# Performance work log

Hardware: AMD Instinct MI355X
Metric: run time of the kernel (lower is better)

The kernel has to match this reference:

```python
import jax, jax.numpy as jnp
import numpy as np

MAX_LEN = 366

def _pe_table(d_model, max_len=MAX_LEN):
    # standard sinusoidal positional encoding table [max_len, d_model]
    pos = jnp.arange(max_len, dtype=jnp.float32)[:, None]
    div = jnp.exp(jnp.arange(0, d_model, 2, dtype=jnp.float32) * (-jnp.log(10000.0) / d_model))
    ang = pos * div  # [max_len, d_model/2]
    pe = jnp.zeros((max_len, d_model), dtype=jnp.float32)
    pe = pe.at[:, 0::2].set(jnp.sin(ang))
    pe = pe.at[:, 1::2].set(jnp.cos(ang))
    return pe

def setup_inputs() -> dict:
    key = jax.random.key(0)
    k1, k2, k3, k4 = jax.random.split(key, 4)
    B, S, F, D = 1024, 128, 10, 256
    input_sequence = jax.random.normal(k1, (B, S, F), dtype=jnp.float32)
    doy_sequence = jnp.sort(jax.random.randint(k2, (B, S), 0, MAX_LEN), axis=-1)
    W = jax.random.normal(k3, (D, F), dtype=jnp.float32) * (1.0 / np.sqrt(F))
    b = jax.random.normal(k4, (D,), dtype=jnp.float32) * 0.01
    return {"input_sequence": input_sequence, "doy_sequence": doy_sequence, "W": W, "b": b}

def reference(input_sequence, doy_sequence, W, b):
    # obs_embed: linear projection of per-observation features  [B,S,D]
    obs_embed = jnp.einsum('bsf,df->bsd', input_sequence, W) + b
    D = W.shape[0]
    pe = _pe_table(D)[doy_sequence]  # vectorized gather over the whole batch [B,S,D]
    # original: x = obs_embed.repeat(1,1,2) then overwrite second half with PE
    out = jnp.concatenate([obs_embed, pe], axis=-1)  # [B,S,2D]
    # dropout is identity in eval mode
    return out
```

## Files before the change

kernel.cpp:

```cpp
#include <hip/hip_runtime.h>


__global__ __launch_bounds__(256) void bert_embed_kernel(
    const float* __restrict__ x,
    const int*   __restrict__ doy,
    const float* __restrict__ W,
    const float* __restrict__ bvec,
    float*       __restrict__ out,
    int BS)
{
    const int lane = threadIdx.x & 63;
    const int wave = threadIdx.x >> 6;
    const int p = blockIdx.x * 4 + wave;
    if (p >= BS) return;

    const float2* xp = (const float2*)(x + (size_t)p * 10);
    float xf[10];
    #pragma unroll
    for (int c = 0; c < 5; ++c) {
        float2 v = xp[c];
        xf[2 * c]     = v.x;
        xf[2 * c + 1] = v.y;
    }

    const int d0 = lane * 4;

    float4 bv = *(const float4*)(bvec + d0);
    float acc[4] = {bv.x, bv.y, bv.z, bv.w};

    {
        const float4* wp = (const float4*)(W + (size_t)d0 * 10);
        float wf[40];
        #pragma unroll
        for (int c = 0; c < 10; ++c) {
            float4 v = wp[c];
            wf[4 * c + 0] = v.x; wf[4 * c + 1] = v.y;
            wf[4 * c + 2] = v.z; wf[4 * c + 3] = v.w;
        }
        #pragma unroll
        for (int r = 0; r < 4; ++r) {
            #pragma unroll
            for (int f = 0; f < 10; ++f)
                acc[r] = fmaf(xf[f], wf[10 * r + f], acc[r]);
        }
    }

    const float pos = (float)doy[p];
    float pe[4];
    #pragma unroll
    for (int q = 0; q < 2; ++q) {
        float j = (float)(2 * lane + q);
        float e = __builtin_amdgcn_exp2f(
            fmaf(j, -0.10381025296522976f, -2.651496129472319f));
        float rev = pos * e;
        float fr = rev - floorf(rev);
        pe[2 * q]     = __builtin_amdgcn_sinf(fr);
        pe[2 * q + 1] = __builtin_amdgcn_cosf(fr);
    }

    float* o = out + (size_t)p * 512;
    float4 s0 = {acc[0], acc[1], acc[2], acc[3]};
    float4 s1 = {pe[0],  pe[1],  pe[2],  pe[3]};
    *(float4*)(o + d0)       = s0;
    *(float4*)(o + 256 + d0) = s1;
}

extern "C" void kernel_launch(void* const* d_in, const int* in_sizes, int n_in,
                              void* d_out, int out_size, void* d_ws, size_t ws_size,
                              hipStream_t stream) {
    const float* x    = (const float*)d_in[0];
    const int*   doy  = (const int*)d_in[1];
    const float* W    = (const float*)d_in[2];
    const float* bvec = (const float*)d_in[3];
    float*       out  = (float*)d_out;

    const int BS = in_sizes[1];
    const int blocks = (BS + 3) / 4;
    bert_embed_kernel<<<blocks, 256, 0, stream>>>(x, doy, W, bvec, out, BS);
}
```

Measured before the change: 318.5 us.

## Process 32 positions per wave, reusing W, bias and PE frequencies in registers

Each wavefront now handles a chunk of 32 consecutive positions instead of one. The W slice, bias and the two exponential frequency terms are loaded or computed once and kept in registers across the chunk. The doy values are loaded in one coalesced read and handed out with shuffles. This cuts redundant W loads and per-position setup, but it shrinks the grid by 32x (about 1024 blocks) and serializes the writes within each wave, which may lower memory-level parallelism on this write-bound kernel.

Result: faster. 280.4 us (-12.0%).

```diff
diff --git a/kernel.cpp b/kernel.cpp
--- a/kernel.cpp
+++ b/kernel.cpp
@@ -1,5 +1,7 @@
 #include <hip/hip_runtime.h>
 
+
+#define CHUNK 32
 
 __global__ __launch_bounds__(256) void bert_embed_kernel(
     const float* __restrict__ x,
@@ -11,58 +13,70 @@
 {
     const int lane = threadIdx.x & 63;
     const int wave = threadIdx.x >> 6;
-    const int p = blockIdx.x * 4 + wave;
-    if (p >= BS) return;
-
-    const float2* xp = (const float2*)(x + (size_t)p * 10);
-    float xf[10];
-    #pragma unroll
-    for (int c = 0; c < 5; ++c) {
-        float2 v = xp[c];
-        xf[2 * c]     = v.x;
-        xf[2 * c + 1] = v.y;
-    }
+    const int gw   = blockIdx.x * 4 + wave;
+    const int base = gw * CHUNK;
+    if (base >= BS) return;
 
     const int d0 = lane * 4;
 
-    float4 bv = *(const float4*)(bvec + d0);
-    float acc[4] = {bv.x, bv.y, bv.z, bv.w};
-
+    float wf[40];
     {
         const float4* wp = (const float4*)(W + (size_t)d0 * 10);
-        float wf[40];
         #pragma unroll
         for (int c = 0; c < 10; ++c) {
             float4 v = wp[c];
             wf[4 * c + 0] = v.x; wf[4 * c + 1] = v.y;
             wf[4 * c + 2] = v.z; wf[4 * c + 3] = v.w;
         }
-        #pragma unroll
-        for (int r = 0; r < 4; ++r) {
-            #pragma unroll
-            for (int f = 0; f < 10; ++f)
-                acc[r] = fmaf(xf[f], wf[10 * r + f], acc[r]);
-        }
     }
 
-    const float pos = (float)doy[p];
-    float pe[4];
-    #pragma unroll
-    for (int q = 0; q < 2; ++q) {
-        float j = (float)(2 * lane + q);
-        float e = __builtin_amdgcn_exp2f(
-            fmaf(j, -0.10381025296522976f, -2.651496129472319f));
-        float rev = pos * e;
-        float fr = rev - floorf(rev);
-        pe[2 * q]     = __builtin_amdgcn_sinf(fr);
-        pe[2 * q + 1] = __builtin_amdgcn_cosf(fr);
+    const float4 bv = *(const float4*)(bvec + d0);
+
+    const float e0 = __builtin_amdgcn_exp2f(
+        fmaf((float)(2 * lane + 0), -0.10381025296522976f, -2.651496129472319f));
+    const float e1 = __builtin_amdgcn_exp2f(
+        fmaf((float)(2 * lane + 1), -0.10381025296522976f, -2.651496129472319f));
+
+    int myDoy = 0;
+    if (lane < CHUNK && base + lane < BS) myDoy = doy[base + lane];
+
+    const int n = min(CHUNK, BS - base);
+    float* o = out + (size_t)base * 512 + d0;
+
+    for (int it = 0; it < n; ++it) {
+        const int p = base + it;
+
+        const float2* xp = (const float2*)(x + (size_t)p * 10);
+        float xf[10];
+        #pragma unroll
+        for (int c = 0; c < 5; ++c) {
+            float2 v = xp[c];
+            xf[2 * c]     = v.x;
+            xf[2 * c + 1] = v.y;
+        }
+
+        float acc0 = bv.x, acc1 = bv.y, acc2 = bv.z, acc3 = bv.w;
+        #pragma unroll
+        for (int f = 0; f < 10; ++f) {
+            acc0 = fmaf(xf[f], wf[ 0 + f], acc0);
+            acc1 = fmaf(xf[f], wf[10 + f], acc1);
+            acc2 = fmaf(xf[f], wf[20 + f], acc2);
+            acc3 = fmaf(xf[f], wf[30 + f], acc3);
+        }
+
+        const float pos = (float)__shfl(myDoy, it);
+        float r0 = pos * e0;
+        float r1 = pos * e1;
+        r0 -= floorf(r0);
+        r1 -= floorf(r1);
+        float4 s1 = { __builtin_amdgcn_sinf(r0), __builtin_amdgcn_cosf(r0),
+                      __builtin_amdgcn_sinf(r1), __builtin_amdgcn_cosf(r1) };
+        float4 s0 = { acc0, acc1, acc2, acc3 };
+
+        *(float4*)(o)       = s0;
+        *(float4*)(o + 256) = s1;
+        o += 512;
     }
-
-    float* o = out + (size_t)p * 512;
-    float4 s0 = {acc[0], acc[1], acc[2], acc[3]};
-    float4 s1 = {pe[0],  pe[1],  pe[2],  pe[3]};
-    *(float4*)(o + d0)       = s0;
-    *(float4*)(o + 256 + d0) = s1;
 }
 
 extern "C" void kernel_launch(void* const* d_in, const int* in_sizes, int n_in,
@@ -75,6 +89,7 @@
     float*       out  = (float*)d_out;
 
     const int BS = in_sizes[1];
-    const int blocks = (BS + 3) / 4;
+    const int waves  = (BS + CHUNK - 1) / CHUNK;
+    const int blocks = (waves + 3) / 4;
     bert_embed_kernel<<<blocks, 256, 0, stream>>>(x, doy, W, bvec, out, BS);
 }
```
